# Kernel optimization log

Hardware: AMD Instinct MI355X
Metric: run time of the kernel (lower is better)

The kernel has to match this reference:

```python
import jax, jax.numpy as jnp
import numpy as np

N = 144      # Lx*Ly lattice sites (12x12)
NH = 256     # GRU hidden units
K = 2        # local Hilbert dim (occupied/empty)
LOG_EPS = 1e-10


def _gru_step(h, x, kernel, rec_kernel, bias):
    # Keras GRU cell, reset_after=True, gate order (z, r, h)
    gx = x @ kernel + bias[0]        # [B, 3*NH]
    gh = h @ rec_kernel + bias[1]    # [B, 3*NH]
    xz, xr, xh = jnp.split(gx, 3, axis=-1)
    hz, hr, hn = jnp.split(gh, 3, axis=-1)
    z = jax.nn.sigmoid(xz + hz)
    r = jax.nn.sigmoid(xr + hr)
    hh = jnp.tanh(xh + r * hn)
    return z * h + (1.0 - z) * hh


def setup_inputs() -> dict:
    key = jax.random.key(0)
    k1, k2, k3 = jax.random.split(key, 3)
    glorot = lambda k, shape: jax.random.uniform(
        k, shape, jnp.float32,
        -jnp.sqrt(6.0 / (shape[0] + shape[1])),
        jnp.sqrt(6.0 / (shape[0] + shape[1])))
    return {
        "kernel": glorot(k1, (K, 3 * NH)),
        "rec_kernel": glorot(k2, (NH, 3 * NH)),
        "bias": jnp.zeros((2, 3 * NH), jnp.float32),
        "dense_w": glorot(k3, (NH, K)),
        "dense_b": jnp.zeros((K,), jnp.float32),
        "nsamples": 1024,
    }


def reference(kernel, rec_kernel, bias, dense_w, dense_b, nsamples):
    h0 = jnp.zeros((nsamples, NH), jnp.float32)
    x0 = jnp.zeros((nsamples, K), jnp.float32)   # 0.0 * one_hot(0)
    logP0 = jnp.zeros((nsamples,), jnp.float32)
    keys = jax.random.split(jax.random.key(42), N)

    def step(carry, step_key):
        h, x, logP = carry
        h = _gru_step(h, x, kernel, rec_kernel, bias)
        probs = jax.nn.softmax(h @ dense_w + dense_b)          # [B, K]
        log_probs = jnp.log(LOG_EPS + probs)                   # matches tf.math.log(1e-10+p)
        s = jax.random.categorical(step_key, log_probs)        # [B] int
        x_new = jax.nn.one_hot(s, K, dtype=jnp.float32)
        logP = logP + jnp.take_along_axis(log_probs, s[:, None], axis=1)[:, 0]
        return (h, x_new, logP), s

    (_, _, logP), samples = jax.lax.scan(step, (h0, x0, logP0), keys)
    samples = samples.T  # [nsamples, N]
    return samples, logP
```

## Files before the change

### kernel.cpp

```cpp
#include <hip/hip_runtime.h>
#include <stdint.h>

#define N_SITES 144
#define NHID    256
#define NSAMP   1024
#define MB      4
#define TPB     768
#define PARTITIONABLE 1

__device__ __forceinline__ uint32_t rotl32(uint32_t v, uint32_t r) {
    return (v << r) | (v >> (32u - r));
}

__device__ __forceinline__ void threefry(uint32_t k0, uint32_t k1,
                                         uint32_t x0, uint32_t x1,
                                         uint32_t& o0, uint32_t& o1) {
    uint32_t ks0 = k0, ks1 = k1, ks2 = k0 ^ k1 ^ 0x1BD11BDAu;
    x0 += ks0; x1 += ks1;
#define RG4(a,b,c,d) \
    x0 += x1; x1 = rotl32(x1,a); x1 ^= x0; \
    x0 += x1; x1 = rotl32(x1,b); x1 ^= x0; \
    x0 += x1; x1 = rotl32(x1,c); x1 ^= x0; \
    x0 += x1; x1 = rotl32(x1,d); x1 ^= x0;
    RG4(13,15,26,6)  x0 += ks1; x1 += ks2 + 1u;
    RG4(17,29,16,24) x0 += ks2; x1 += ks0 + 2u;
    RG4(13,15,26,6)  x0 += ks0; x1 += ks1 + 3u;
    RG4(17,29,16,24) x0 += ks1; x1 += ks2 + 4u;
    RG4(13,15,26,6)  x0 += ks2; x1 += ks0 + 5u;
#undef RG4
    o0 = x0; o1 = x1;
}

__device__ __forceinline__ float gumbel_from_bits(uint32_t bits) {
#pragma clang fp contract(off)
    const float TINY = 1.17549435e-38f;
    uint32_t fb = (bits >> 9) | 0x3f800000u;
    float u = __uint_as_float(fb) - 1.0f;
    u = u * (1.0f - TINY) + TINY;
    u = fmaxf(TINY, u);
    return -logf(-logf(u));
}

__global__ __launch_bounds__(TPB, 1)
void rnn_sample_kernel(const float* __restrict__ kern,
                       const float* __restrict__ rec,
                       const float* __restrict__ bias,
                       const float* __restrict__ dw,
                       const float* __restrict__ db,
                       float* __restrict__ out)
{
    const int t    = threadIdx.x;
    const int blk  = blockIdx.x;
    const int b0   = blk * MB;
    const int wv   = t >> 6;
    const int lane = t & 63;

    __shared__ float4   hs4[NHID];
    __shared__ float    pacc[MB][TPB];
    __shared__ uint32_t keyA[N_SITES], keyB[N_SITES];
    __shared__ float    wred[4][8];
    __shared__ int      sPrev[MB];
    __shared__ float    lgP[MB];

    float kz0 = 0.f, kr0 = 0.f, kn0 = 0.f, kz1 = 0.f, kr1 = 0.f, kn1 = 0.f;
    float b0z = 0.f, b0r = 0.f, b0n = 0.f, b1z = 0.f, b1r = 0.f, b1n = 0.f;
    float dwa = 0.f, dwb = 0.f, dba = 0.f, dbb = 0.f;
    if (t < NHID) {
        const int c0 = t, c1 = t + 256, c2 = t + 512;
        kz0 = kern[c0];       kr0 = kern[c1];       kn0 = kern[c2];
        kz1 = kern[768 + c0]; kr1 = kern[768 + c1]; kn1 = kern[768 + c2];
        b0z = bias[c0];       b0r = bias[c1];       b0n = bias[c2];
        b1z = bias[768 + c0]; b1r = bias[768 + c1]; b1n = bias[768 + c2];
        dwa = dw[2 * t];      dwb = dw[2 * t + 1];
        dba = db[0];          dbb = db[1];
        hs4[t] = make_float4(0.f, 0.f, 0.f, 0.f);
    }
    if (t < MB) { sPrev[t] = -1; lgP[t] = 0.f; }
    if (t < N_SITES) {
        uint32_t o0, o1;
        threefry(0u, 42u, 0u, (uint32_t)t, o0, o1);
        keyA[t] = o0; keyB[t] = o1;
    }
    __syncthreads();

    for (int n = 0; n < N_SITES; ++n) {
        float a0 = 0.f, a1 = 0.f, a2 = 0.f, a3 = 0.f;
        {
            const float* rp = rec + t;
#pragma unroll 8
            for (int k = 0; k < NHID; ++k) {
                float4 h4 = hs4[k];
                float w  = rp[0];
                rp += 768;
                a0 = fmaf(h4.x, w, a0);
                a1 = fmaf(h4.y, w, a1);
                a2 = fmaf(h4.z, w, a2);
                a3 = fmaf(h4.w, w, a3);
            }
        }
        pacc[0][t] = a0; pacc[1][t] = a1; pacc[2][t] = a2; pacc[3][t] = a3;
        __syncthreads();

        float hnew[MB];
        if (t < NHID) {
            float4 ho = hs4[t];
            float hold[MB] = { ho.x, ho.y, ho.z, ho.w };
            {
#pragma clang fp contract(off)
#pragma unroll
                for (int m = 0; m < MB; ++m) {
                    const int sp = sPrev[m];
                    float xz = (sp == 0) ? kz0 : ((sp == 1) ? kz1 : 0.f);
                    float xr = (sp == 0) ? kr0 : ((sp == 1) ? kr1 : 0.f);
                    float xh = (sp == 0) ? kn0 : ((sp == 1) ? kn1 : 0.f);
                    xz = xz + b0z;  xr = xr + b0r;  xh = xh + b0n;
                    const float hz = pacc[m][t]       + b1z;
                    const float hr = pacc[m][t + 256] + b1r;
                    const float hn = pacc[m][t + 512] + b1n;
                    const float z = 1.0f / (1.0f + expf(-(xz + hz)));
                    const float r = 1.0f / (1.0f + expf(-(xr + hr)));
                    const float rhn = r * hn;
                    const float hh = tanhf(xh + rhn);
                    hnew[m] = z * hold[m] + (1.0f - z) * hh;
                }
            }
            hs4[t] = make_float4(hnew[0], hnew[1], hnew[2], hnew[3]);

#pragma unroll
            for (int m = 0; m < MB; ++m) {
                float va = hnew[m] * dwa;
                float vb = hnew[m] * dwb;
#pragma unroll
                for (int off = 32; off > 0; off >>= 1) {
                    va += __shfl_xor(va, off, 64);
                    vb += __shfl_xor(vb, off, 64);
                }
                if (lane == 0) { wred[wv][2 * m] = va; wred[wv][2 * m + 1] = vb; }
            }
        }
        __syncthreads();

        if (t < MB) {
            const int m = t;
            float l0 = wred[0][2 * m] + wred[1][2 * m] + wred[2][2 * m] + wred[3][2 * m];
            float l1 = wred[0][2 * m + 1] + wred[1][2 * m + 1] + wred[2][2 * m + 1] + wred[3][2 * m + 1];
            uint32_t o0a, o1a, o0b, o1b;
            const uint32_t fbase = 2u * (uint32_t)(b0 + m);
            threefry(keyA[n], keyB[n], 0u, fbase,      o0a, o1a);
            threefry(keyA[n], keyB[n], 0u, fbase + 1u, o0b, o1b);
            const float g0 = gumbel_from_bits(o0a ^ o1a);
            const float g1 = gumbel_from_bits(o0b ^ o1b);
            {
#pragma clang fp contract(off)
                l0 = l0 + dba;
                l1 = l1 + dbb;
                const float mx = fmaxf(l0, l1);
                const float e0 = expf(l0 - mx), e1 = expf(l1 - mx);
                const float den = e0 + e1;
                const float lp0 = logf(1e-10f + e0 / den);
                const float lp1 = logf(1e-10f + e1 / den);
                const float v0 = g0 + lp0;
                const float v1 = g1 + lp1;
                const int s = (v1 > v0) ? 1 : 0;
                sPrev[m] = s;
                lgP[m] = lgP[m] + (s ? lp1 : lp0);
                out[(size_t)(b0 + m) * N_SITES + n] = (float)s;
            }
        }
        __syncthreads();
    }

    if (t < MB) out[(size_t)NSAMP * N_SITES + (b0 + t)] = lgP[t];
}

extern "C" void kernel_launch(void* const* d_in, const int* in_sizes, int n_in,
                              void* d_out, int out_size, void* d_ws, size_t ws_size,
                              hipStream_t stream) {
    (void)in_sizes; (void)n_in; (void)d_ws; (void)ws_size; (void)out_size;
    const float* kern = (const float*)d_in[0];
    const float* rec  = (const float*)d_in[1];
    const float* bias = (const float*)d_in[2];
    const float* dwp  = (const float*)d_in[3];
    const float* dbp  = (const float*)d_in[4];
    float* out = (float*)d_out;
    rnn_sample_kernel<<<NSAMP / MB, TPB, 0, stream>>>(kern, rec, bias, dwp, dbp, out);
}
```

Measured before the change: 1.573 ms.

## Broadcast hidden state via scalar loads from global memory instead of LDS

Moves the per-block hidden state out of shared memory into a global buffer, and reads it in the matvec with s_load_dwordx16 into scalar registers after invalidating the scalar cache each step. Every FMA then uses a uniform SGPR operand instead of an LDS float4 read. The old hidden value is also kept in a register rather than reloaded. The risks are coherence between vector stores and scalar loads through global memory, a serializing s_waitcnt on each 16-row chunk, and removing the unroll of the weight-load loop.

```diff
diff --git a/kernel.cpp b/kernel.cpp
--- a/kernel.cpp
+++ b/kernel.cpp
@@ -7,6 +7,10 @@
 #define MB      4
 #define TPB     768
 #define PARTITIONABLE 1
+
+__device__ float4 g_h[NSAMP / MB][NHID];
+
+typedef float f32x16 __attribute__((ext_vector_type(16)));
 
 __device__ __forceinline__ uint32_t rotl32(uint32_t v, uint32_t r) {
     return (v << r) | (v >> (32u - r));
@@ -55,16 +59,19 @@
     const int wv   = t >> 6;
     const int lane = t & 63;
 
-    __shared__ float4   hs4[NHID];
     __shared__ float    pacc[MB][TPB];
     __shared__ uint32_t keyA[N_SITES], keyB[N_SITES];
     __shared__ float    wred[4][8];
     __shared__ int      sPrev[MB];
     __shared__ float    lgP[MB];
 
+    float4* __restrict__ hg = &g_h[blk][0];
+    const uint64_t hbase = (uint64_t)(uintptr_t)hg;
+
     float kz0 = 0.f, kr0 = 0.f, kn0 = 0.f, kz1 = 0.f, kr1 = 0.f, kn1 = 0.f;
     float b0z = 0.f, b0r = 0.f, b0n = 0.f, b1z = 0.f, b1r = 0.f, b1n = 0.f;
     float dwa = 0.f, dwb = 0.f, dba = 0.f, dbb = 0.f;
+    float hreg[MB] = { 0.f, 0.f, 0.f, 0.f };
     if (t < NHID) {
         const int c0 = t, c1 = t + 256, c2 = t + 512;
         kz0 = kern[c0];       kr0 = kern[c1];       kn0 = kern[c2];
@@ -73,7 +80,7 @@
         b1z = bias[768 + c0]; b1r = bias[768 + c1]; b1n = bias[768 + c2];
         dwa = dw[2 * t];      dwb = dw[2 * t + 1];
         dba = db[0];          dbb = db[1];
-        hs4[t] = make_float4(0.f, 0.f, 0.f, 0.f);
+        hg[t] = make_float4(0.f, 0.f, 0.f, 0.f);
     }
     if (t < MB) { sPrev[t] = -1; lgP[t] = 0.f; }
     if (t < N_SITES) {
@@ -85,17 +92,31 @@
 
     for (int n = 0; n < N_SITES; ++n) {
         float a0 = 0.f, a1 = 0.f, a2 = 0.f, a3 = 0.f;
+        asm volatile("s_waitcnt lgkmcnt(0)\n\ts_dcache_inv" ::: "memory");
         {
-            const float* rp = rec + t;
-#pragma unroll 8
-            for (int k = 0; k < NHID; ++k) {
-                float4 h4 = hs4[k];
-                float w  = rp[0];
-                rp += 768;
-                a0 = fmaf(h4.x, w, a0);
-                a1 = fmaf(h4.y, w, a1);
-                a2 = fmaf(h4.z, w, a2);
-                a3 = fmaf(h4.w, w, a3);
+            const float* rcol = rec + t;
+#pragma unroll 1
+            for (int k0 = 0; k0 < NHID; k0 += 16) {
+                f32x16 h0v, h1v, h2v, h3v;
+                asm volatile(
+                    "s_load_dwordx16 %0, %4, 0x0\n\t"
+                    "s_load_dwordx16 %1, %4, 0x40\n\t"
+                    "s_load_dwordx16 %2, %4, 0x80\n\t"
+                    "s_load_dwordx16 %3, %4, 0xC0\n\t"
+                    "s_waitcnt lgkmcnt(0)"
+                    : "=s"(h0v), "=s"(h1v), "=s"(h2v), "=s"(h3v)
+                    : "s"(hbase + (uint64_t)k0 * 16u));
+                const float* rp = rcol + (size_t)k0 * 768;
+#define FMA1(HV, I, KOFF) { \
+                const float w = rp[(size_t)(KOFF + I) * 768]; \
+                a0 = fmaf(HV[4*I+0], w, a0); \
+                a1 = fmaf(HV[4*I+1], w, a1); \
+                a2 = fmaf(HV[4*I+2], w, a2); \
+                a3 = fmaf(HV[4*I+3], w, a3); }
+#define FMA4(HV, KOFF) FMA1(HV,0,KOFF) FMA1(HV,1,KOFF) FMA1(HV,2,KOFF) FMA1(HV,3,KOFF)
+                FMA4(h0v, 0) FMA4(h1v, 4) FMA4(h2v, 8) FMA4(h3v, 12)
+#undef FMA4
+#undef FMA1
             }
         }
         pacc[0][t] = a0; pacc[1][t] = a1; pacc[2][t] = a2; pacc[3][t] = a3;
@@ -103,8 +124,6 @@
 
         float hnew[MB];
         if (t < NHID) {
-            float4 ho = hs4[t];
-            float hold[MB] = { ho.x, ho.y, ho.z, ho.w };
             {
 #pragma clang fp contract(off)
 #pragma unroll
@@ -121,10 +140,11 @@
                     const float r = 1.0f / (1.0f + expf(-(xr + hr)));
                     const float rhn = r * hn;
                     const float hh = tanhf(xh + rhn);
-                    hnew[m] = z * hold[m] + (1.0f - z) * hh;
+                    hnew[m] = z * hreg[m] + (1.0f - z) * hh;
+                    hreg[m] = hnew[m];
                 }
             }
-            hs4[t] = make_float4(hnew[0], hnew[1], hnew[2], hnew[3]);
+            hg[t] = make_float4(hnew[0], hnew[1], hnew[2], hnew[3]);
 
 #pragma unroll
             for (int m = 0; m < MB; ++m) {
```

Result: slower. 1.633 ms (+3.8%).

## Cache recurrent weights in registers and precompute Gumbel noise before the scan

Applied to the files above, without the earlier changes.

Each thread now keeps the first 96 rows of its recurrent-weight column in registers, so each step reloads only the remaining rows from global memory. All per-step Gumbel noise is generated in parallel before the loop and stored in shared memory. The previous hidden state is kept in registers, and the trailing per-step barrier is removed. The launch bound is also raised to 3 blocks per CU. That bound tightens the register budget and may force the 96-entry weight cache to spill to scratch. With one block per CU in this grid, the extra occupancy does not buy anything.

```diff
diff --git a/kernel.cpp b/kernel.cpp
--- a/kernel.cpp
+++ b/kernel.cpp
@@ -6,6 +6,7 @@
 #define NSAMP   1024
 #define MB      4
 #define TPB     768
+#define PREC    96
 #define PARTITIONABLE 1
 
 __device__ __forceinline__ uint32_t rotl32(uint32_t v, uint32_t r) {
@@ -41,7 +42,7 @@
     return -logf(-logf(u));
 }
 
-__global__ __launch_bounds__(TPB, 1)
+__global__ __launch_bounds__(TPB, 3)
 void rnn_sample_kernel(const float* __restrict__ kern,
                        const float* __restrict__ rec,
                        const float* __restrict__ bias,
@@ -58,18 +59,24 @@
     __shared__ float4   hs4[NHID];
     __shared__ float    pacc[MB][TPB];
     __shared__ uint32_t keyA[N_SITES], keyB[N_SITES];
+    __shared__ float    glds[N_SITES][MB][2];
     __shared__ float    wred[4][8];
     __shared__ int      sPrev[MB];
     __shared__ float    lgP[MB];
 
+    float wreg[PREC];
+#pragma unroll
+    for (int r = 0; r < PREC; ++r) wreg[r] = rec[(size_t)r * 768 + t];
+
     float kz0 = 0.f, kr0 = 0.f, kn0 = 0.f, kz1 = 0.f, kr1 = 0.f, kn1 = 0.f;
     float b0z = 0.f, b0r = 0.f, b0n = 0.f, b1z = 0.f, b1r = 0.f, b1n = 0.f;
     float dwa = 0.f, dwb = 0.f, dba = 0.f, dbb = 0.f;
+    float hreg[MB] = { 0.f, 0.f, 0.f, 0.f };
     if (t < NHID) {
         const int c0 = t, c1 = t + 256, c2 = t + 512;
         kz0 = kern[c0];       kr0 = kern[c1];       kn0 = kern[c2];
+        b0z = bias[c0];       b0r = bias[c1];       b0n = bias[c2];
         kz1 = kern[768 + c0]; kr1 = kern[768 + c1]; kn1 = kern[768 + c2];
-        b0z = bias[c0];       b0r = bias[c1];       b0n = bias[c2];
         b1z = bias[768 + c0]; b1r = bias[768 + c1]; b1n = bias[768 + c2];
         dwa = dw[2 * t];      dwb = dw[2 * t + 1];
         dba = db[0];          dbb = db[1];
@@ -83,12 +90,31 @@
     }
     __syncthreads();
 
+    if (t < N_SITES * MB) {
+        const int n = t >> 2, m = t & 3;
+        uint32_t o0a, o1a, o0b, o1b;
+        const uint32_t fbase = 2u * (uint32_t)(b0 + m);
+        threefry(keyA[n], keyB[n], 0u, fbase,      o0a, o1a);
+        threefry(keyA[n], keyB[n], 0u, fbase + 1u, o0b, o1b);
+        glds[n][m][0] = gumbel_from_bits(o0a ^ o1a);
+        glds[n][m][1] = gumbel_from_bits(o0b ^ o1b);
+    }
+    __syncthreads();
+
     for (int n = 0; n < N_SITES; ++n) {
         float a0 = 0.f, a1 = 0.f, a2 = 0.f, a3 = 0.f;
         {
-            const float* rp = rec + t;
-#pragma unroll 8
-            for (int k = 0; k < NHID; ++k) {
+#pragma unroll
+            for (int k = 0; k < PREC; ++k) {
+                float4 h4 = hs4[k];
+                a0 = fmaf(h4.x, wreg[k], a0);
+                a1 = fmaf(h4.y, wreg[k], a1);
+                a2 = fmaf(h4.z, wreg[k], a2);
+                a3 = fmaf(h4.w, wreg[k], a3);
+            }
+            const float* rp = rec + (size_t)PREC * 768 + t;
+#pragma unroll 16
+            for (int k = PREC; k < NHID; ++k) {
                 float4 h4 = hs4[k];
                 float w  = rp[0];
                 rp += 768;
@@ -103,8 +129,6 @@
 
         float hnew[MB];
         if (t < NHID) {
-            float4 ho = hs4[t];
-            float hold[MB] = { ho.x, ho.y, ho.z, ho.w };
             {
 #pragma clang fp contract(off)
 #pragma unroll
@@ -121,7 +145,8 @@
                     const float r = 1.0f / (1.0f + expf(-(xr + hr)));
                     const float rhn = r * hn;
                     const float hh = tanhf(xh + rhn);
-                    hnew[m] = z * hold[m] + (1.0f - z) * hh;
+                    hnew[m] = z * hreg[m] + (1.0f - z) * hh;
+                    hreg[m] = hnew[m];
                 }
             }
             hs4[t] = make_float4(hnew[0], hnew[1], hnew[2], hnew[3]);
@@ -144,12 +169,8 @@
             const int m = t;
             float l0 = wred[0][2 * m] + wred[1][2 * m] + wred[2][2 * m] + wred[3][2 * m];
             float l1 = wred[0][2 * m + 1] + wred[1][2 * m + 1] + wred[2][2 * m + 1] + wred[3][2 * m + 1];
-            uint32_t o0a, o1a, o0b, o1b;
-            const uint32_t fbase = 2u * (uint32_t)(b0 + m);
-            threefry(keyA[n], keyB[n], 0u, fbase,      o0a, o1a);
-            threefry(keyA[n], keyB[n], 0u, fbase + 1u, o0b, o1b);
-            const float g0 = gumbel_from_bits(o0a ^ o1a);
-            const float g1 = gumbel_from_bits(o0b ^ o1b);
+            const float g0 = glds[n][m][0];
+            const float g1 = glds[n][m][1];
             {
 #pragma clang fp contract(off)
                 l0 = l0 + dba;
@@ -167,9 +188,9 @@
                 out[(size_t)(b0 + m) * N_SITES + n] = (float)s;
             }
         }
-        __syncthreads();
-    }
-
+    }
+
+    __syncthreads();
     if (t < MB) out[(size_t)NSAMP * N_SITES + (b0 + t)] = lgP[t];
 }
 
```

New measurement: 5.558 ms. 3.53x slower.

## Transpose recurrent weights, precompute Gumbel noise, keep hidden state in registers

Applied to the files above, without the earlier changes.

A pre-pass kernel transposes the recurrent weight matrix into workspace so each thread can stream its own column as contiguous float4 loads. All Gumbel noise for every site is now generated once before the sequential loop instead of on four threads each step. The old hidden state and the log-probability accumulator stay in registers, and the trailing barrier of each step is dropped. The main risk is that per-thread contiguous rows are strided across lanes, which can hurt coalescing and cache behaviour compared with the original column-coalesced reads.

```diff
diff --git a/kernel.cpp b/kernel.cpp
--- a/kernel.cpp
+++ b/kernel.cpp
@@ -41,6 +41,14 @@
     return -logf(-logf(u));
 }
 
+__global__ void transpose_rec(const float* __restrict__ rec,
+                              float* __restrict__ recT) {
+    const int col = blockIdx.x;
+    const int k   = threadIdx.x;
+    recT[(size_t)col * NHID + k] = rec[(size_t)k * TPB + col];
+}
+
+template <bool TRANS>
 __global__ __launch_bounds__(TPB, 1)
 void rnn_sample_kernel(const float* __restrict__ kern,
                        const float* __restrict__ rec,
@@ -58,13 +66,15 @@
     __shared__ float4   hs4[NHID];
     __shared__ float    pacc[MB][TPB];
     __shared__ uint32_t keyA[N_SITES], keyB[N_SITES];
+    __shared__ float    glds[N_SITES][MB][2];
     __shared__ float    wred[4][8];
     __shared__ int      sPrev[MB];
-    __shared__ float    lgP[MB];
 
     float kz0 = 0.f, kr0 = 0.f, kn0 = 0.f, kz1 = 0.f, kr1 = 0.f, kn1 = 0.f;
     float b0z = 0.f, b0r = 0.f, b0n = 0.f, b1z = 0.f, b1r = 0.f, b1n = 0.f;
     float dwa = 0.f, dwb = 0.f, dba = 0.f, dbb = 0.f;
+    float hreg[MB] = { 0.f, 0.f, 0.f, 0.f };
+    float lgPr = 0.f;
     if (t < NHID) {
         const int c0 = t, c1 = t + 256, c2 = t + 512;
         kz0 = kern[c0];       kr0 = kern[c1];       kn0 = kern[c2];
@@ -75,7 +85,7 @@
         dba = db[0];          dbb = db[1];
         hs4[t] = make_float4(0.f, 0.f, 0.f, 0.f);
     }
-    if (t < MB) { sPrev[t] = -1; lgP[t] = 0.f; }
+    if (t < MB) sPrev[t] = -1;
     if (t < N_SITES) {
         uint32_t o0, o1;
         threefry(0u, 42u, 0u, (uint32_t)t, o0, o1);
@@ -83,15 +93,43 @@
     }
     __syncthreads();
 
+    if (t < N_SITES * MB) {
+        const int n = t >> 2, m = t & 3;
+        uint32_t o0a, o1a, o0b, o1b;
+        const uint32_t fbase = 2u * (uint32_t)(b0 + m);
+        threefry(keyA[n], keyB[n], 0u, fbase,      o0a, o1a);
+        threefry(keyA[n], keyB[n], 0u, fbase + 1u, o0b, o1b);
+        glds[n][m][0] = gumbel_from_bits(o0a ^ o1a);
+        glds[n][m][1] = gumbel_from_bits(o0b ^ o1b);
+    }
+    __syncthreads();
+
     for (int n = 0; n < N_SITES; ++n) {
         float a0 = 0.f, a1 = 0.f, a2 = 0.f, a3 = 0.f;
-        {
+        if (TRANS) {
+            const float* rt = rec + (size_t)t * NHID;
+#pragma unroll 4
+            for (int k0 = 0; k0 < NHID; k0 += 16) {
+                const float4 w0 = *reinterpret_cast<const float4*>(rt + k0 + 0);
+                const float4 w1 = *reinterpret_cast<const float4*>(rt + k0 + 4);
+                const float4 w2 = *reinterpret_cast<const float4*>(rt + k0 + 8);
+                const float4 w3 = *reinterpret_cast<const float4*>(rt + k0 + 12);
+#define KSTEP(W, J) { const float4 h4 = hs4[k0 + (J)]; \
+                a0 = fmaf(h4.x, (W), a0); a1 = fmaf(h4.y, (W), a1); \
+                a2 = fmaf(h4.z, (W), a2); a3 = fmaf(h4.w, (W), a3); }
+                KSTEP(w0.x,  0) KSTEP(w0.y,  1) KSTEP(w0.z,  2) KSTEP(w0.w,  3)
+                KSTEP(w1.x,  4) KSTEP(w1.y,  5) KSTEP(w1.z,  6) KSTEP(w1.w,  7)
+                KSTEP(w2.x,  8) KSTEP(w2.y,  9) KSTEP(w2.z, 10) KSTEP(w2.w, 11)
+                KSTEP(w3.x, 12) KSTEP(w3.y, 13) KSTEP(w3.z, 14) KSTEP(w3.w, 15)
+#undef KSTEP
+            }
+        } else {
             const float* rp = rec + t;
 #pragma unroll 8
             for (int k = 0; k < NHID; ++k) {
                 float4 h4 = hs4[k];
                 float w  = rp[0];
-                rp += 768;
+                rp += TPB;
                 a0 = fmaf(h4.x, w, a0);
                 a1 = fmaf(h4.y, w, a1);
                 a2 = fmaf(h4.z, w, a2);
@@ -103,8 +141,6 @@
 
         float hnew[MB];
         if (t < NHID) {
-            float4 ho = hs4[t];
-            float hold[MB] = { ho.x, ho.y, ho.z, ho.w };
             {
 #pragma clang fp contract(off)
 #pragma unroll
@@ -121,7 +157,8 @@
                     const float r = 1.0f / (1.0f + expf(-(xr + hr)));
                     const float rhn = r * hn;
                     const float hh = tanhf(xh + rhn);
-                    hnew[m] = z * hold[m] + (1.0f - z) * hh;
+                    hnew[m] = z * hreg[m] + (1.0f - z) * hh;
+                    hreg[m] = hnew[m];
                 }
             }
             hs4[t] = make_float4(hnew[0], hnew[1], hnew[2], hnew[3]);
@@ -144,12 +181,8 @@
             const int m = t;
             float l0 = wred[0][2 * m] + wred[1][2 * m] + wred[2][2 * m] + wred[3][2 * m];
             float l1 = wred[0][2 * m + 1] + wred[1][2 * m + 1] + wred[2][2 * m + 1] + wred[3][2 * m + 1];
-            uint32_t o0a, o1a, o0b, o1b;
-            const uint32_t fbase = 2u * (uint32_t)(b0 + m);
-            threefry(keyA[n], keyB[n], 0u, fbase,      o0a, o1a);
-            threefry(keyA[n], keyB[n], 0u, fbase + 1u, o0b, o1b);
-            const float g0 = gumbel_from_bits(o0a ^ o1a);
-            const float g1 = gumbel_from_bits(o0b ^ o1b);
+            const float g0 = glds[n][m][0];
+            const float g1 = glds[n][m][1];
             {
 #pragma clang fp contract(off)
                 l0 = l0 + dba;
@@ -163,25 +196,32 @@
                 const float v1 = g1 + lp1;
                 const int s = (v1 > v0) ? 1 : 0;
                 sPrev[m] = s;
-                lgP[m] = lgP[m] + (s ? lp1 : lp0);
+                lgPr = lgPr + (s ? lp1 : lp0);
                 out[(size_t)(b0 + m) * N_SITES + n] = (float)s;
             }
         }
-        __syncthreads();
-    }
-
-    if (t < MB) out[(size_t)NSAMP * N_SITES + (b0 + t)] = lgP[t];
+    }
+
+    if (t < MB) out[(size_t)NSAMP * N_SITES + (b0 + t)] = lgPr;
 }
 
 extern "C" void kernel_launch(void* const* d_in, const int* in_sizes, int n_in,
                               void* d_out, int out_size, void* d_ws, size_t ws_size,
                               hipStream_t stream) {
-    (void)in_sizes; (void)n_in; (void)d_ws; (void)ws_size; (void)out_size;
+    (void)in_sizes; (void)n_in; (void)out_size;
     const float* kern = (const float*)d_in[0];
     const float* rec  = (const float*)d_in[1];
     const float* bias = (const float*)d_in[2];
     const float* dwp  = (const float*)d_in[3];
     const float* dbp  = (const float*)d_in[4];
     float* out = (float*)d_out;
-    rnn_sample_kernel<<<NSAMP / MB, TPB, 0, stream>>>(kern, rec, bias, dwp, dbp, out);
-}
+
+    const size_t needT = sizeof(float) * (size_t)NHID * TPB;
+    if (d_ws != nullptr && ws_size >= needT) {
+        float* recT = (float*)d_ws;
+        transpose_rec<<<TPB, NHID, 0, stream>>>(rec, recT);
+        rnn_sample_kernel<true><<<NSAMP / MB, TPB, 0, stream>>>(kern, recT, bias, dwp, dbp, out);
+    } else {
+        rnn_sample_kernel<false><<<NSAMP / MB, TPB, 0, stream>>>(kern, rec, bias, dwp, dbp, out);
+    }
+}
```

Result: slower. 3.376 ms (+114.6%).
